# Optimization experiments

Measured on AMD Instinct MI355X. Metric: run time of the kernel, lower is better.

Reference implementation:

```python
import jax, jax.numpy as jnp
import numpy as np

T, N, F, E, P, G, H, B = 8, 40000, 256, 640000, 128, 128, 128, 1024

def setup_inputs() -> dict:
    key = jax.random.key(0)
    ks = jax.random.split(key, 20)
    s = 0.05
    inp = {
        "x": jax.random.normal(ks[0], (T, N, F), jnp.float32),
        "edge_index": jax.random.randint(ks[1], (2, E), 0, N, dtype=jnp.int64),
        "target_indices": jax.random.randint(ks[2], (B,), 0, N, dtype=jnp.int64),
        # projection layer
        "proj_w": jax.random.normal(ks[3], (F, P), jnp.float32) * s,
        "proj_b": jnp.zeros((P,), jnp.float32),
        # GCN layers (weight + bias, symmetric-norm GCNConv with self-loops)
        "gcn_w1": jax.random.normal(ks[4], (P, G), jnp.float32) * s,
        "gcn_b1": jnp.zeros((G,), jnp.float32),
        "gcn_w2": jax.random.normal(ks[5], (G, G), jnp.float32) * s,
        "gcn_b2": jnp.zeros((G,), jnp.float32),
        # GRU (PyTorch layout: [3H, in], gates order r,z,n)
        "gru_w_ih": jax.random.normal(ks[6], (3 * H, 2 * G), jnp.float32) * s,
        "gru_w_hh": jax.random.normal(ks[7], (3 * H, H), jnp.float32) * s,
        "gru_b_ih": jnp.zeros((3 * H,), jnp.float32),
        "gru_b_hh": jnp.zeros((3 * H,), jnp.float32),
        # attention pooling
        "attn_w": jax.random.normal(ks[8], (H, 1), jnp.float32) * s,
        "attn_b": jnp.zeros((1,), jnp.float32),
        # predictor MLP (dropout in eval mode -> identity)
        "pred_w1": jax.random.normal(ks[9], (H, 16), jnp.float32) * s,
        "pred_b1": jnp.zeros((16,), jnp.float32),
        "pred_w2": jax.random.normal(ks[10], (16, 1), jnp.float32) * s,
        "pred_b2": jnp.zeros((1,), jnp.float32),
    }
    return inp


def reference(x, edge_index, target_indices, proj_w, proj_b, gcn_w1, gcn_b1,
              gcn_w2, gcn_b2, gru_w_ih, gru_w_hh, gru_b_ih, gru_b_hh,
              attn_w, attn_b, pred_w1, pred_b1, pred_w2, pred_b2):
    n = x.shape[1]
    # GCNConv normalization: add self-loops, deg^-1/2 A_hat deg^-1/2
    loops = jnp.arange(n, dtype=edge_index.dtype)
    src = jnp.concatenate([edge_index[0], loops])
    dst = jnp.concatenate([edge_index[1], loops])
    deg = jax.ops.segment_sum(jnp.ones_like(src, x.dtype), dst, num_segments=n)
    dinv = jnp.where(deg > 0, jax.lax.rsqrt(deg), 0.0)
    norm = (dinv[src] * dinv[dst])[:, None]  # [E+N, 1]

    def gcn_layer(h, w, b):
        m = h @ w                               # [N, G]
        agg = jax.ops.segment_sum(m[src] * norm, dst, num_segments=n)
        return jax.nn.relu(agg + b)

    def per_step(xt):
        h = jax.nn.relu(xt @ proj_w + proj_b)    # projection
        h1 = gcn_layer(h, gcn_w1, gcn_b1)
        h2 = gcn_layer(h1, gcn_w2, gcn_b2)
        return jnp.concatenate([h1, h2], axis=-1)  # jumping-knowledge concat

    emb = jax.vmap(per_step)(x)                  # [T, N, 2G]
    tgt = emb[:, target_indices]                 # [T, B, 2G]

    hdim = gru_w_hh.shape[1]
    def gru_cell(h, xt):
        gi = xt @ gru_w_ih.T + gru_b_ih
        gh = h @ gru_w_hh.T + gru_b_hh
        ir, iz, ig = jnp.split(gi, 3, axis=-1)
        hr, hz, hg = jnp.split(gh, 3, axis=-1)
        r = jax.nn.sigmoid(ir + hr)
        z = jax.nn.sigmoid(iz + hz)
        g = jnp.tanh(ig + r * hg)
        h_new = (1.0 - z) * g + z * h
        return h_new, h_new

    h0 = jnp.zeros((tgt.shape[1], hdim), x.dtype)
    _, outs = jax.lax.scan(gru_cell, h0, tgt)    # [T, B, H]
    rnn_out = outs.transpose(1, 0, 2)            # [B, T, H]

    scores = jnp.tanh(rnn_out @ attn_w + attn_b)       # [B, T, 1]
    attn_weights = jax.nn.softmax(scores, axis=1)
    rep = jnp.sum(rnn_out * attn_weights, axis=1)      # [B, H]

    hmid = jax.nn.relu(rep @ pred_w1 + pred_b1)        # dropout: eval mode
    pred = hmid @ pred_w2 + pred_b2                    # [B, 1]
    return pred, attn_weights.squeeze(-1)
```

## Files before the change

kernel.cpp:

```cpp
#include <hip/hip_runtime.h>
#include <stdint.h>

#define TT 8
#define NN 40000
#define FF 256
#define EE 640000
#define BB 1024
#define ROWS 320000

typedef __attribute__((ext_vector_type(8))) short s16x8;
typedef __attribute__((ext_vector_type(4))) float f32x4;

__device__ __forceinline__ unsigned short f2bf(float f){
  unsigned int u = __float_as_uint(f);
  u += 0x7fffu + ((u >> 16) & 1u);
  return (unsigned short)(u >> 16);
}
__device__ __forceinline__ float bflo(unsigned int u){ return __uint_as_float(u << 16); }
__device__ __forceinline__ float bfhi(unsigned int u){ return __uint_as_float(u & 0xffff0000u); }

__device__ __forceinline__ void gl2lds16(const void* g, void* l){
  auto gp = reinterpret_cast<const unsigned int __attribute__((address_space(1)))*>(
      reinterpret_cast<uintptr_t>(g));
  auto lp = reinterpret_cast<unsigned int __attribute__((address_space(3)))*>(
      static_cast<unsigned int>(reinterpret_cast<uintptr_t>(l)));
  __builtin_amdgcn_global_load_lds(gp, lp, 16, 0, 0);
}

__global__ void prep_k(const float* __restrict__ proj_w, const float* __restrict__ w1,
                       const float* __restrict__ w2, const float* __restrict__ wih,
                       const float* __restrict__ whh,
                       unsigned short* __restrict__ projwt, unsigned short* __restrict__ w1t,
                       unsigned short* __restrict__ w2t, unsigned short* __restrict__ wihb,
                       uint2* __restrict__ whhp)
{
  int i = blockIdx.x * 256 + threadIdx.x;
  if (i < 32768) {
    int p = i >> 8, f = i & 255;
    projwt[i] = f2bf(proj_w[f * 128 + p]);
  } else if (i < 49152) {
    int k = i - 32768; int o = k >> 7, c = k & 127;
    w1t[k] = f2bf(w1[c * 128 + o]);
  } else if (i < 65536) {
    int k = i - 49152; int o = k >> 7, c = k & 127;
    w2t[k] = f2bf(w2[c * 128 + o]);
  } else if (i < 163840) {
    int k = i - 65536;
    wihb[k] = f2bf(wih[k]);
  } else if (i < 180224) {
    int k = i - 163840; int kk = k >> 7, j = k & 127;
    unsigned int lo = (unsigned int)f2bf(whh[j * 128 + kk]) |
                      ((unsigned int)f2bf(whh[(128 + j) * 128 + kk]) << 16);
    unsigned int hi = (unsigned int)f2bf(whh[(256 + j) * 128 + kk]);
    whhp[k] = make_uint2(lo, hi);
  }
}

__global__ void init_k(int* __restrict__ counts, int* __restrict__ fill){
  int i = blockIdx.x * 256 + threadIdx.x;
  if (i < NN) { counts[i] = 0; fill[i] = 0; }
}
__global__ void count_k(const int* __restrict__ dst, int* __restrict__ counts){
  int i = blockIdx.x * 256 + threadIdx.x;
  if (i < EE) atomicAdd(&counts[dst[i]], 1);
}
__global__ void scan_k(const int* __restrict__ counts, int* __restrict__ rp,
                       float* __restrict__ dinv)
{
  __shared__ int sums[1024];
  const int CH = 40;
  int t = threadIdx.x;
  int beg = t * CH, end = beg + CH; if (end > NN) end = NN; if (beg > NN) beg = NN;
  int s = 0;
  for (int i = beg; i < end; i++) s += counts[i];
  sums[t] = s;
  __syncthreads();
  for (int off = 1; off < 1024; off <<= 1) {
    int add = (t >= off) ? sums[t - off] : 0;
    __syncthreads();
    sums[t] += add;
    __syncthreads();
  }
  int run = sums[t] - s;
  for (int i = beg; i < end; i++) { rp[i] = run; run += counts[i]; }
  if (t == 1023) rp[NN] = sums[1023];
  for (int i = beg; i < end; i++) dinv[i] = rsqrtf((float)(counts[i] + 1));
}
__global__ void fill_k(const int* __restrict__ src, const int* __restrict__ dst,
                       const int* __restrict__ rp, int* __restrict__ fill,
                       int* __restrict__ ci)
{
  int i = blockIdx.x * 256 + threadIdx.x;
  if (i < EE) {
    int d = dst[i];
    int pos = rp[d] + atomicAdd(&fill[d], 1);
    ci[pos] = src[i];
  }
}

template<int MODE>
__global__ __launch_bounds__(256)
void gemm_k(const void* __restrict__ Ap, const short* __restrict__ Bt,
            void* __restrict__ Cp, int K, int ldc,
            const float* __restrict__ dinv)
{
  __shared__ short lA[128 * 64];
  __shared__ short lB[128 * 64];
  const int tid = threadIdx.x;
  const int lane = tid & 63, wave = tid >> 6;
  const int row0 = blockIdx.x * 128;
  const int col0 = blockIdx.y * 128;
  const int qr = (wave & 1) * 64, qc = (wave >> 1) * 64;
  const int m = lane & 15, q = lane >> 4;

  f32x4 acc[4][4];
#pragma unroll
  for (int i = 0; i < 4; i++)
#pragma unroll
    for (int j = 0; j < 4; j++) acc[i][j] = (f32x4){0.f, 0.f, 0.f, 0.f};

  for (int k0 = 0; k0 < K; k0 += 64) {
    __syncthreads();
    {
      const short* A = (const short*)Ap;
#pragma unroll
      for (int i = 0; i < 4; i++) {
        int c = wave * 4 + i;
        int row = c * 8 + (lane >> 3);
        int kg = (lane & 7) ^ (row & 7);
        gl2lds16(A + (size_t)(row0 + row) * K + k0 + kg * 8, lA + c * 512);
      }
    }
#pragma unroll
    for (int i = 0; i < 4; i++) {
      int c = wave * 4 + i;
      int row = c * 8 + (lane >> 3);
      int kg = (lane & 7) ^ (row & 7);
      gl2lds16(Bt + (size_t)(col0 + row) * K + k0 + kg * 8, lB + c * 512);
    }
    __syncthreads();
#pragma unroll
    for (int ks = 0; ks < 2; ks++) {
      s16x8 af[4], bf[4];
#pragma unroll
      for (int i = 0; i < 4; i++) {
        int R = qr + 16 * i + m;
        af[i] = *(const s16x8*)&lA[R * 64 + (((ks * 4 + q) ^ (R & 7)) * 8)];
        int RB = qc + 16 * i + m;
        bf[i] = *(const s16x8*)&lB[RB * 64 + (((ks * 4 + q) ^ (RB & 7)) * 8)];
      }
#pragma unroll
      for (int i = 0; i < 4; i++)
#pragma unroll
        for (int j = 0; j < 4; j++)
          acc[i][j] = __builtin_amdgcn_mfma_f32_16x16x32_bf16(af[i], bf[j], acc[i][j], 0, 0, 0);
    }
  }
#pragma unroll
  for (int i = 0; i < 4; i++) {
    int rbase = row0 + qr + 16 * i + q * 4;
#pragma unroll
    for (int j = 0; j < 4; j++) {
      int col = col0 + qc + 16 * j + m;
#pragma unroll
      for (int rr = 0; rr < 4; rr++) {
        int rg = rbase + rr;
        float v = acc[i][j][rr];
        if (MODE == 1) {
          v *= dinv[rg % NN];
          ((unsigned short*)Cp)[(size_t)rg * ldc + col] = f2bf(v);
        } else {
          ((float*)Cp)[(size_t)rg * ldc + col] = v;
        }
      }
    }
  }
}

__global__ __launch_bounds__(256)
void projgcn_k(const float* __restrict__ x, const short* __restrict__ projwt,
               const short* __restrict__ w1t, const float* __restrict__ proj_b,
               const float* __restrict__ dinv, unsigned short* __restrict__ Ms1)
{
  __shared__ short lds[128 * 64 * 3];
  short* lA = lds;
  short* lB = lds + 8192;
  short* lH = lds + 8192;
  const int tid = threadIdx.x;
  const int lane = tid & 63, wave = tid >> 6;
  const int row0 = blockIdx.x * 128;
  const int qr = (wave & 1) * 64, qc = (wave >> 1) * 64;
  const int m = lane & 15, q = lane >> 4;

  f32x4 acc[4][4];
#pragma unroll
  for (int i = 0; i < 4; i++)
#pragma unroll
    for (int j = 0; j < 4; j++) acc[i][j] = (f32x4){0.f, 0.f, 0.f, 0.f};

  for (int k0 = 0; k0 < 256; k0 += 64) {
    __syncthreads();
    {
      int row = tid >> 1, half = tid & 1;
      const float* gp = x + (size_t)(row0 + row) * 256 + k0 + half * 32;
#pragma unroll
      for (int gi = 0; gi < 4; gi++) {
        float4 v0 = *(const float4*)(gp + gi * 8);
        float4 v1 = *(const float4*)(gp + gi * 8 + 4);
        uint4 w;
        w.x = (unsigned)f2bf(v0.x) | ((unsigned)f2bf(v0.y) << 16);
        w.y = (unsigned)f2bf(v0.z) | ((unsigned)f2bf(v0.w) << 16);
        w.z = (unsigned)f2bf(v1.x) | ((unsigned)f2bf(v1.y) << 16);
        w.w = (unsigned)f2bf(v1.z) | ((unsigned)f2bf(v1.w) << 16);
        int g = half * 4 + gi;
        *(uint4*)&lA[row * 64 + ((g ^ (row & 7)) * 8)] = w;
      }
    }
#pragma unroll
    for (int i = 0; i < 4; i++) {
      int c = wave * 4 + i;
      int row = c * 8 + (lane >> 3);
      int kg = (lane & 7) ^ (row & 7);
      gl2lds16(projwt + (size_t)row * 256 + k0 + kg * 8, lB + c * 512);
    }
    __syncthreads();
#pragma unroll
    for (int ks = 0; ks < 2; ks++) {
      s16x8 af[4], bf[4];
#pragma unroll
      for (int i = 0; i < 4; i++) {
        int R = qr + 16 * i + m;
        af[i] = *(const s16x8*)&lA[R * 64 + (((ks * 4 + q) ^ (R & 7)) * 8)];
        int RB = qc + 16 * i + m;
        bf[i] = *(const s16x8*)&lB[RB * 64 + (((ks * 4 + q) ^ (RB & 7)) * 8)];
      }
#pragma unroll
      for (int i = 0; i < 4; i++)
#pragma unroll
        for (int j = 0; j < 4; j++)
          acc[i][j] = __builtin_amdgcn_mfma_f32_16x16x32_bf16(af[i], bf[j], acc[i][j], 0, 0, 0);
    }
  }
  __syncthreads();

#pragma unroll
  for (int i = 0; i < 4; i++) {
    int rb = qr + 16 * i + q * 4;
#pragma unroll
    for (int j = 0; j < 4; j++) {
      int c = qc + 16 * j + m;
      int chalf = c & 64;
      int gsw = (c >> 3) & 7;
      float bv = proj_b[c];
#pragma unroll
      for (int rr = 0; rr < 4; rr++) {
        int r_loc = rb + rr;
        float v = fmaxf(acc[i][j][rr] + bv, 0.f);
        lH[r_loc * 128 + chalf + ((gsw ^ (r_loc & 7)) << 3) + (c & 7)] = (short)f2bf(v);
      }
      acc[i][j] = (f32x4){0.f, 0.f, 0.f, 0.f};
    }
  }

  for (int k0 = 0; k0 < 128; k0 += 64) {
    __syncthreads();
#pragma unroll
    for (int i = 0; i < 4; i++) {
      int c = wave * 4 + i;
      int row = c * 8 + (lane >> 3);
      int kg = (lane & 7) ^ (row & 7);
      gl2lds16(w1t + (size_t)row * 128 + k0 + kg * 8, lA + c * 512);
    }
    __syncthreads();
#pragma unroll
    for (int ks = 0; ks < 2; ks++) {
      s16x8 af[4], bf[4];
#pragma unroll
      for (int i = 0; i < 4; i++) {
        int R = qr + 16 * i + m;
        af[i] = *(const s16x8*)&lH[R * 128 + k0 + (((ks * 4 + q) ^ (R & 7)) << 3)];
        int RB = qc + 16 * i + m;
        bf[i] = *(const s16x8*)&lA[RB * 64 + (((ks * 4 + q) ^ (RB & 7)) << 3)];
      }
#pragma unroll
      for (int i = 0; i < 4; i++)
#pragma unroll
        for (int j = 0; j < 4; j++)
          acc[i][j] = __builtin_amdgcn_mfma_f32_16x16x32_bf16(af[i], bf[j], acc[i][j], 0, 0, 0);
    }
  }

#pragma unroll
  for (int i = 0; i < 4; i++) {
    int rbase = row0 + qr + 16 * i + q * 4;
#pragma unroll
    for (int j = 0; j < 4; j++) {
      int col = qc + 16 * j + m;
#pragma unroll
      for (int rr = 0; rr < 4; rr++) {
        int rg = rbase + rr;
        float v = acc[i][j][rr] * dinv[rg % NN];
        Ms1[(size_t)rg * 128 + col] = f2bf(v);
      }
    }
  }
}

__global__ __launch_bounds__(256)
void agg_k(const uint2* __restrict__ Ms, uint2* __restrict__ Hout,
           const int* __restrict__ rp, const int* __restrict__ ci,
           const float* __restrict__ dinv, const float* __restrict__ bias)
{
  int widx = blockIdx.x * 4 + (threadIdx.x >> 6);
  int lane = threadIdx.x & 63;
  int li = lane & 31, h = lane >> 5;
  int t = widx / NN;
  int v = widx - t * NN;
  const uint2* base = Ms + (size_t)t * NN * 32 + li;

  uint2 su = base[(size_t)v * 32];
  float a0, a1, a2, a3;
  if (h == 0) { a0 = bflo(su.x); a1 = bfhi(su.x); a2 = bflo(su.y); a3 = bfhi(su.y); }
  else        { a0 = 0.f; a1 = 0.f; a2 = 0.f; a3 = 0.f; }

  int e0 = rp[v], e1 = rp[v + 1];
  for (int chunk = e0; chunk < e1; chunk += 64) {
    int cnt = min(64, e1 - chunk);
    int myIdx = (lane < cnt) ? ci[chunk + lane] : 0;
    int j = 0;
    for (; j + 8 <= cnt; j += 8) {
      int s0 = __shfl(myIdx, j + h, 64);
      int s1 = __shfl(myIdx, j + 2 + h, 64);
      int s2 = __shfl(myIdx, j + 4 + h, 64);
      int s3 = __shfl(myIdx, j + 6 + h, 64);
      uint2 w0 = base[(size_t)s0 * 32];
      uint2 w1 = base[(size_t)s1 * 32];
      uint2 w2 = base[(size_t)s2 * 32];
      uint2 w3 = base[(size_t)s3 * 32];
      a0 += bflo(w0.x) + bflo(w1.x) + bflo(w2.x) + bflo(w3.x);
      a1 += bfhi(w0.x) + bfhi(w1.x) + bfhi(w2.x) + bfhi(w3.x);
      a2 += bflo(w0.y) + bflo(w1.y) + bflo(w2.y) + bflo(w3.y);
      a3 += bfhi(w0.y) + bfhi(w1.y) + bfhi(w2.y) + bfhi(w3.y);
    }
    for (; j + 2 <= cnt; j += 2) {
      int s = __shfl(myIdx, j + h, 64);
      uint2 w = base[(size_t)s * 32];
      a0 += bflo(w.x); a1 += bfhi(w.x); a2 += bflo(w.y); a3 += bfhi(w.y);
    }
    if (j < cnt) {
      int s = __shfl(myIdx, j, 64);
      if (h == 0) {
        uint2 w = base[(size_t)s * 32];
        a0 += bflo(w.x); a1 += bfhi(w.x); a2 += bflo(w.y); a3 += bfhi(w.y);
      }
    }
  }
  a0 += __shfl_xor(a0, 32, 64);
  a1 += __shfl_xor(a1, 32, 64);
  a2 += __shfl_xor(a2, 32, 64);
  a3 += __shfl_xor(a3, 32, 64);
  if (h == 0) {
    float dv = dinv[v];
    float r0 = fmaxf(fmaf(dv, a0, bias[li * 4 + 0]), 0.f);
    float r1 = fmaxf(fmaf(dv, a1, bias[li * 4 + 1]), 0.f);
    float r2 = fmaxf(fmaf(dv, a2, bias[li * 4 + 2]), 0.f);
    float r3 = fmaxf(fmaf(dv, a3, bias[li * 4 + 3]), 0.f);
    uint2 o;
    o.x = (unsigned)f2bf(r0) | ((unsigned)f2bf(r1) << 16);
    o.y = (unsigned)f2bf(r2) | ((unsigned)f2bf(r3) << 16);
    Hout[(size_t)widx * 32 + li] = o;
  }
}

__global__ void gather_k(const unsigned int* __restrict__ h1, const unsigned int* __restrict__ h2,
                         const int* __restrict__ tix, unsigned int* __restrict__ TGT)
{
  int i = blockIdx.x * 256 + threadIdx.x;
  int dw = i & 127; int r = i >> 7; int b = r & 1023; int t = r >> 10;
  int node = tix[b];
  size_t src = ((size_t)t * NN + node) * 64 + (dw & 63);
  unsigned int val = (dw < 64) ? h1[src] : h2[src];
  TGT[(size_t)r * 128 + dw] = val;
}

__global__ __launch_bounds__(256)
void gru_attn_k(const float* __restrict__ GI, const uint2* __restrict__ Whp,
                const float* __restrict__ b_ih, const float* __restrict__ b_hh,
                const float* __restrict__ attw, const float* __restrict__ attb,
                float* __restrict__ rep, float* __restrict__ out_attn)
{
  __shared__ float hbuf[2][128];
  __shared__ float red[2][2];
  __shared__ float sc[2][8];
  int tid = threadIdx.x;
  int r = tid >> 7, j = tid & 127;
  int lane = tid & 63, wv = tid >> 6;
  int b = blockIdx.x * 2 + r;
  hbuf[r][j] = 0.f;
  float bi0 = b_ih[j], bi1 = b_ih[128 + j], bi2 = b_ih[256 + j];
  float bh0 = b_hh[j], bh1 = b_hh[128 + j], bh2 = b_hh[256 + j];
  float aw = attw[j], ab = attb[0];
  float ht[8];
  __syncthreads();
  for (int t = 0; t < 8; t++) {
    const float* gi = GI + ((size_t)(t * 1024 + b)) * 384;
    float accr = bh0, accz = bh1, accg = bh2;
#pragma unroll 4
    for (int k = 0; k < 128; k++) {
      float hk = hbuf[r][k];
      uint2 wp = Whp[k * 128 + j];
      accr += hk * bflo(wp.x);
      accz += hk * bfhi(wp.x);
      accg += hk * bflo(wp.y);
    }
    float x0 = gi[j] + bi0, x1 = gi[128 + j] + bi1, x2 = gi[256 + j] + bi2;
    float rg = 1.f / (1.f + __expf(-(x0 + accr)));
    float z  = 1.f / (1.f + __expf(-(x1 + accz)));
    float g  = tanhf(x2 + rg * accg);
    float hp = hbuf[r][j];
    float hn = (1.f - z) * g + z * hp;
    __syncthreads();
    hbuf[r][j] = hn;
    float p = hn * aw;
    for (int off = 32; off; off >>= 1) p += __shfl_down(p, off, 64);
    if (lane == 0) red[wv >> 1][wv & 1] = p;
    __syncthreads();
    if (j == 0) sc[r][t] = tanhf(red[r][0] + red[r][1] + ab);
    ht[t] = hn;
  }
  __syncthreads();
  float s[8], mx = -1e30f;
#pragma unroll
  for (int t = 0; t < 8; t++) { s[t] = sc[r][t]; mx = fmaxf(mx, s[t]); }
  float sum = 0.f;
#pragma unroll
  for (int t = 0; t < 8; t++) { s[t] = __expf(s[t] - mx); sum += s[t]; }
  float inv = 1.f / sum;
  float rv = 0.f;
#pragma unroll
  for (int t = 0; t < 8; t++) rv += s[t] * inv * ht[t];
  rep[(size_t)b * 128 + j] = rv;
  if (j < 8) out_attn[b * 8 + j] = s[j] * inv;
}

__global__ void pred_k(const float* __restrict__ rep, const float* __restrict__ w1,
                       const float* __restrict__ b1, const float* __restrict__ w2,
                       const float* __restrict__ b2, float* __restrict__ out)
{
  int bidx = blockIdx.x * 256 + threadIdx.x;
  if (bidx >= 1024) return;
  const float* rp = rep + (size_t)bidx * 128;
  float acc[16];
#pragma unroll
  for (int i = 0; i < 16; i++) acc[i] = b1[i];
  for (int k = 0; k < 128; k++) {
    float rv = rp[k];
#pragma unroll
    for (int i = 0; i < 16; i++) acc[i] += rv * w1[k * 16 + i];
  }
  float pv = b2[0];
#pragma unroll
  for (int i = 0; i < 16; i++) pv += fmaxf(acc[i], 0.f) * w2[i];
  out[bidx] = pv;
}

extern "C" void kernel_launch(void* const* d_in, const int* in_sizes, int n_in,
                              void* d_out, int out_size, void* d_ws, size_t ws_size,
                              hipStream_t stream)
{
  (void)in_sizes; (void)n_in; (void)out_size; (void)ws_size;
  const float* x      = (const float*)d_in[0];
  const int*   ei     = (const int*)d_in[1];
  const int*   tix    = (const int*)d_in[2];
  const float* proj_w = (const float*)d_in[3];
  const float* proj_b = (const float*)d_in[4];
  const float* gcn_w1 = (const float*)d_in[5];
  const float* gcn_b1 = (const float*)d_in[6];
  const float* gcn_w2 = (const float*)d_in[7];
  const float* gcn_b2 = (const float*)d_in[8];
  const float* w_ih   = (const float*)d_in[9];
  const float* w_hh   = (const float*)d_in[10];
  const float* b_ih   = (const float*)d_in[11];
  const float* b_hh   = (const float*)d_in[12];
  const float* attw   = (const float*)d_in[13];
  const float* attb   = (const float*)d_in[14];
  const float* pw1    = (const float*)d_in[15];
  const float* pb1    = (const float*)d_in[16];
  const float* pw2    = (const float*)d_in[17];
  const float* pb2    = (const float*)d_in[18];
  float* out = (float*)d_out;

  char* ws = (char*)d_ws;
  size_t off = 0;
  auto alloc = [&](size_t bytes) -> char* {
    char* p = ws + off; off += (bytes + 255) & ~(size_t)255; return p;
  };
  int*   counts = (int*)alloc((size_t)NN * 4);
  int*   fill   = (int*)alloc((size_t)NN * 4);
  int*   rp     = (int*)alloc((size_t)(NN + 1) * 4);
  float* dinv   = (float*)alloc((size_t)NN * 4);
  int*   ci     = (int*)alloc((size_t)EE * 4);
  unsigned short* projwt = (unsigned short*)alloc(128 * 256 * 2);
  unsigned short* w1t    = (unsigned short*)alloc(128 * 128 * 2);
  unsigned short* w2t    = (unsigned short*)alloc(128 * 128 * 2);
  unsigned short* wihb   = (unsigned short*)alloc(384 * 256 * 2);
  uint2* whhp            = (uint2*)alloc(128 * 128 * 8);
  unsigned int* TGT = (unsigned int*)alloc((size_t)8192 * 256 * 2);
  float* GI  = (float*)alloc((size_t)8192 * 384 * 4);
  float* rep = (float*)alloc((size_t)1024 * 128 * 4);
  unsigned short* bufA = (unsigned short*)alloc((size_t)ROWS * 128 * 2);
  unsigned short* bufB = (unsigned short*)alloc((size_t)ROWS * 128 * 2);
  unsigned short* bufC = (unsigned short*)alloc((size_t)ROWS * 128 * 2);

  const int* e_src = ei;
  const int* e_dst = ei + EE;

  prep_k<<<704, 256, 0, stream>>>(proj_w, gcn_w1, gcn_w2, w_ih, w_hh,
                                  projwt, w1t, w2t, wihb, whhp);
  init_k<<<157, 256, 0, stream>>>(counts, fill);
  count_k<<<2500, 256, 0, stream>>>(e_dst, counts);
  scan_k<<<1, 1024, 0, stream>>>(counts, rp, dinv);
  fill_k<<<2500, 256, 0, stream>>>(e_src, e_dst, rp, fill, ci);

  projgcn_k<<<2500, 256, 0, stream>>>(x, (const short*)projwt, (const short*)w1t,
                                      proj_b, dinv, bufB);
  agg_k<<<80000, 256, 0, stream>>>((const uint2*)bufB, (uint2*)bufC,
                                   rp, ci, dinv, gcn_b1);
  gemm_k<1><<<dim3(2500, 1), 256, 0, stream>>>(bufC, (const short*)w2t, bufB,
                                               128, 128, dinv);
  agg_k<<<80000, 256, 0, stream>>>((const uint2*)bufB, (uint2*)bufA,
                                   rp, ci, dinv, gcn_b2);
  gather_k<<<4096, 256, 0, stream>>>((const unsigned int*)bufC, (const unsigned int*)bufA,
                                     tix, TGT);
  gemm_k<2><<<dim3(64, 3), 256, 0, stream>>>(TGT, (const short*)wihb, GI,
                                             256, 384, nullptr);
  gru_attn_k<<<512, 256, 0, stream>>>(GI, whhp, b_ih, b_hh, attw, attb, rep, out + 1024);
  pred_k<<<4, 256, 0, stream>>>(rep, pw1, pb1, pw2, pb2, out);
}
```

Measured before the change: 1.172 ms.

## Widen aggregation loads to 16 bytes and fuse gather, init, and predictor kernels

The sparse aggregation kernel now has 16 lanes each load a 16-byte (8 bf16) slice of a row, so a wave processes four neighbours per step instead of two. The target-row gather is folded into the GRU input GEMM through indexed global-to-LDS loads, which removes the TGT buffer and one launch. The counter init is merged into the prep kernel, and the prediction MLP is merged into the GRU/attention kernel. The wider loads cut the number of memory instructions in the dominant aggregation pass, but the extra shuffle reduction stages and the remainder handling add some overhead.

```diff
diff --git a/kernel.cpp b/kernel.cpp
--- a/kernel.cpp
+++ b/kernel.cpp
@@ -32,9 +32,10 @@
                        const float* __restrict__ whh,
                        unsigned short* __restrict__ projwt, unsigned short* __restrict__ w1t,
                        unsigned short* __restrict__ w2t, unsigned short* __restrict__ wihb,
-                       uint2* __restrict__ whhp)
+                       uint2* __restrict__ whhp, int* __restrict__ counts, int* __restrict__ fill)
 {
   int i = blockIdx.x * 256 + threadIdx.x;
+  if (i < NN) { counts[i] = 0; fill[i] = 0; }
   if (i < 32768) {
     int p = i >> 8, f = i & 255;
     projwt[i] = f2bf(proj_w[f * 128 + p]);
@@ -56,10 +57,6 @@
   }
 }
 
-__global__ void init_k(int* __restrict__ counts, int* __restrict__ fill){
-  int i = blockIdx.x * 256 + threadIdx.x;
-  if (i < NN) { counts[i] = 0; fill[i] = 0; }
-}
 __global__ void count_k(const int* __restrict__ dst, int* __restrict__ counts){
   int i = blockIdx.x * 256 + threadIdx.x;
   if (i < EE) atomicAdd(&counts[dst[i]], 1);
@@ -98,11 +95,12 @@
   }
 }
 
-template<int MODE>
+template<int MODE, int GIA>
 __global__ __launch_bounds__(256)
 void gemm_k(const void* __restrict__ Ap, const short* __restrict__ Bt,
             void* __restrict__ Cp, int K, int ldc,
-            const float* __restrict__ dinv)
+            const float* __restrict__ dinv,
+            const short* __restrict__ A2, const int* __restrict__ tix)
 {
   __shared__ short lA[128 * 64];
   __shared__ short lB[128 * 64];
@@ -121,7 +119,20 @@
 
   for (int k0 = 0; k0 < K; k0 += 64) {
     __syncthreads();
-    {
+    if (GIA) {
+      const short* h1p = (const short*)Ap;
+#pragma unroll
+      for (int i = 0; i < 4; i++) {
+        int c = wave * 4 + i;
+        int row = c * 8 + (lane >> 3);
+        int kg = (lane & 7) ^ (row & 7);
+        int r = row0 + row;
+        int tt = r >> 10, bb = r & 1023;
+        int node = tix[bb];
+        const short* srcp = (k0 < 128) ? h1p : A2;
+        gl2lds16(srcp + ((size_t)tt * NN + node) * 128 + (k0 & 127) + kg * 8, lA + c * 512);
+      }
+    } else {
       const short* A = (const short*)Ap;
 #pragma unroll
       for (int i = 0; i < 4; i++) {
@@ -307,87 +318,98 @@
 }
 
 __global__ __launch_bounds__(256)
-void agg_k(const uint2* __restrict__ Ms, uint2* __restrict__ Hout,
+void agg_k(const uint4* __restrict__ Ms, uint4* __restrict__ Hout,
            const int* __restrict__ rp, const int* __restrict__ ci,
            const float* __restrict__ dinv, const float* __restrict__ bias)
 {
   int widx = blockIdx.x * 4 + (threadIdx.x >> 6);
   int lane = threadIdx.x & 63;
-  int li = lane & 31, h = lane >> 5;
+  int li = lane & 15, g = lane >> 4;
   int t = widx / NN;
   int v = widx - t * NN;
-  const uint2* base = Ms + (size_t)t * NN * 32 + li;
-
-  uint2 su = base[(size_t)v * 32];
-  float a0, a1, a2, a3;
-  if (h == 0) { a0 = bflo(su.x); a1 = bfhi(su.x); a2 = bflo(su.y); a3 = bfhi(su.y); }
-  else        { a0 = 0.f; a1 = 0.f; a2 = 0.f; a3 = 0.f; }
+  const uint4* base = Ms + (size_t)t * NN * 16 + li;
+
+  float a0 = 0.f, a1 = 0.f, a2 = 0.f, a3 = 0.f, a4 = 0.f, a5 = 0.f, a6 = 0.f, a7 = 0.f;
+  if (g == 0) {
+    uint4 su = base[(size_t)v * 16];
+    a0 = bflo(su.x); a1 = bfhi(su.x); a2 = bflo(su.y); a3 = bfhi(su.y);
+    a4 = bflo(su.z); a5 = bfhi(su.z); a6 = bflo(su.w); a7 = bfhi(su.w);
+  }
 
   int e0 = rp[v], e1 = rp[v + 1];
   for (int chunk = e0; chunk < e1; chunk += 64) {
     int cnt = min(64, e1 - chunk);
     int myIdx = (lane < cnt) ? ci[chunk + lane] : 0;
     int j = 0;
-    for (; j + 8 <= cnt; j += 8) {
-      int s0 = __shfl(myIdx, j + h, 64);
-      int s1 = __shfl(myIdx, j + 2 + h, 64);
-      int s2 = __shfl(myIdx, j + 4 + h, 64);
-      int s3 = __shfl(myIdx, j + 6 + h, 64);
-      uint2 w0 = base[(size_t)s0 * 32];
-      uint2 w1 = base[(size_t)s1 * 32];
-      uint2 w2 = base[(size_t)s2 * 32];
-      uint2 w3 = base[(size_t)s3 * 32];
+    for (; j + 16 <= cnt; j += 16) {
+      int s0 = __shfl(myIdx, j + g, 64);
+      int s1 = __shfl(myIdx, j + 4 + g, 64);
+      int s2 = __shfl(myIdx, j + 8 + g, 64);
+      int s3 = __shfl(myIdx, j + 12 + g, 64);
+      uint4 w0 = base[(size_t)s0 * 16];
+      uint4 w1 = base[(size_t)s1 * 16];
+      uint4 w2 = base[(size_t)s2 * 16];
+      uint4 w3 = base[(size_t)s3 * 16];
       a0 += bflo(w0.x) + bflo(w1.x) + bflo(w2.x) + bflo(w3.x);
       a1 += bfhi(w0.x) + bfhi(w1.x) + bfhi(w2.x) + bfhi(w3.x);
       a2 += bflo(w0.y) + bflo(w1.y) + bflo(w2.y) + bflo(w3.y);
       a3 += bfhi(w0.y) + bfhi(w1.y) + bfhi(w2.y) + bfhi(w3.y);
-    }
-    for (; j + 2 <= cnt; j += 2) {
-      int s = __shfl(myIdx, j + h, 64);
-      uint2 w = base[(size_t)s * 32];
+      a4 += bflo(w0.z) + bflo(w1.z) + bflo(w2.z) + bflo(w3.z);
+      a5 += bfhi(w0.z) + bfhi(w1.z) + bfhi(w2.z) + bfhi(w3.z);
+      a6 += bflo(w0.w) + bflo(w1.w) + bflo(w2.w) + bflo(w3.w);
+      a7 += bfhi(w0.w) + bfhi(w1.w) + bfhi(w2.w) + bfhi(w3.w);
+    }
+    for (; j + 4 <= cnt; j += 4) {
+      int s = __shfl(myIdx, j + g, 64);
+      uint4 w = base[(size_t)s * 16];
       a0 += bflo(w.x); a1 += bfhi(w.x); a2 += bflo(w.y); a3 += bfhi(w.y);
-    }
-    if (j < cnt) {
-      int s = __shfl(myIdx, j, 64);
-      if (h == 0) {
-        uint2 w = base[(size_t)s * 32];
+      a4 += bflo(w.z); a5 += bfhi(w.z); a6 += bflo(w.w); a7 += bfhi(w.w);
+    }
+    int rem = cnt - j;
+    if (rem > 0) {
+      int sidx = j + g; if (sidx >= cnt) sidx = j;
+      int s = __shfl(myIdx, sidx, 64);
+      if (g < rem) {
+        uint4 w = base[(size_t)s * 16];
         a0 += bflo(w.x); a1 += bfhi(w.x); a2 += bflo(w.y); a3 += bfhi(w.y);
-      }
-    }
-  }
-  a0 += __shfl_xor(a0, 32, 64);
-  a1 += __shfl_xor(a1, 32, 64);
-  a2 += __shfl_xor(a2, 32, 64);
-  a3 += __shfl_xor(a3, 32, 64);
-  if (h == 0) {
+        a4 += bflo(w.z); a5 += bfhi(w.z); a6 += bflo(w.w); a7 += bfhi(w.w);
+      }
+    }
+  }
+  a0 += __shfl_xor(a0, 16, 64); a0 += __shfl_xor(a0, 32, 64);
+  a1 += __shfl_xor(a1, 16, 64); a1 += __shfl_xor(a1, 32, 64);
+  a2 += __shfl_xor(a2, 16, 64); a2 += __shfl_xor(a2, 32, 64);
+  a3 += __shfl_xor(a3, 16, 64); a3 += __shfl_xor(a3, 32, 64);
+  a4 += __shfl_xor(a4, 16, 64); a4 += __shfl_xor(a4, 32, 64);
+  a5 += __shfl_xor(a5, 16, 64); a5 += __shfl_xor(a5, 32, 64);
+  a6 += __shfl_xor(a6, 16, 64); a6 += __shfl_xor(a6, 32, 64);
+  a7 += __shfl_xor(a7, 16, 64); a7 += __shfl_xor(a7, 32, 64);
+  if (g == 0) {
     float dv = dinv[v];
-    float r0 = fmaxf(fmaf(dv, a0, bias[li * 4 + 0]), 0.f);
-    float r1 = fmaxf(fmaf(dv, a1, bias[li * 4 + 1]), 0.f);
-    float r2 = fmaxf(fmaf(dv, a2, bias[li * 4 + 2]), 0.f);
-    float r3 = fmaxf(fmaf(dv, a3, bias[li * 4 + 3]), 0.f);
-    uint2 o;
+    float r0 = fmaxf(fmaf(dv, a0, bias[li * 8 + 0]), 0.f);
+    float r1 = fmaxf(fmaf(dv, a1, bias[li * 8 + 1]), 0.f);
+    float r2 = fmaxf(fmaf(dv, a2, bias[li * 8 + 2]), 0.f);
+    float r3 = fmaxf(fmaf(dv, a3, bias[li * 8 + 3]), 0.f);
+    float r4 = fmaxf(fmaf(dv, a4, bias[li * 8 + 4]), 0.f);
+    float r5 = fmaxf(fmaf(dv, a5, bias[li * 8 + 5]), 0.f);
+    float r6 = fmaxf(fmaf(dv, a6, bias[li * 8 + 6]), 0.f);
+    float r7 = fmaxf(fmaf(dv, a7, bias[li * 8 + 7]), 0.f);
+    uint4 o;
     o.x = (unsigned)f2bf(r0) | ((unsigned)f2bf(r1) << 16);
     o.y = (unsigned)f2bf(r2) | ((unsigned)f2bf(r3) << 16);
-    Hout[(size_t)widx * 32 + li] = o;
-  }
-}
-
-__global__ void gather_k(const unsigned int* __restrict__ h1, const unsigned int* __restrict__ h2,
-                         const int* __restrict__ tix, unsigned int* __restrict__ TGT)
-{
-  int i = blockIdx.x * 256 + threadIdx.x;
-  int dw = i & 127; int r = i >> 7; int b = r & 1023; int t = r >> 10;
-  int node = tix[b];
-  size_t src = ((size_t)t * NN + node) * 64 + (dw & 63);
-  unsigned int val = (dw < 64) ? h1[src] : h2[src];
-  TGT[(size_t)r * 128 + dw] = val;
+    o.z = (unsigned)f2bf(r4) | ((unsigned)f2bf(r5) << 16);
+    o.w = (unsigned)f2bf(r6) | ((unsigned)f2bf(r7) << 16);
+    Hout[(size_t)widx * 16 + li] = o;
+  }
 }
 
 __global__ __launch_bounds__(256)
 void gru_attn_k(const float* __restrict__ GI, const uint2* __restrict__ Whp,
                 const float* __restrict__ b_ih, const float* __restrict__ b_hh,
                 const float* __restrict__ attw, const float* __restrict__ attb,
-                float* __restrict__ rep, float* __restrict__ out_attn)
+                const float* __restrict__ pw1, const float* __restrict__ pb1,
+                const float* __restrict__ pw2, const float* __restrict__ pb2,
+                float* __restrict__ out)
 {
   __shared__ float hbuf[2][128];
   __shared__ float red[2][2];
@@ -439,29 +461,20 @@
   float rv = 0.f;
 #pragma unroll
   for (int t = 0; t < 8; t++) rv += s[t] * inv * ht[t];
-  rep[(size_t)b * 128 + j] = rv;
-  if (j < 8) out_attn[b * 8 + j] = s[j] * inv;
-}
-
-__global__ void pred_k(const float* __restrict__ rep, const float* __restrict__ w1,
-                       const float* __restrict__ b1, const float* __restrict__ w2,
-                       const float* __restrict__ b2, float* __restrict__ out)
-{
-  int bidx = blockIdx.x * 256 + threadIdx.x;
-  if (bidx >= 1024) return;
-  const float* rp = rep + (size_t)bidx * 128;
-  float acc[16];
-#pragma unroll
-  for (int i = 0; i < 16; i++) acc[i] = b1[i];
-  for (int k = 0; k < 128; k++) {
-    float rv = rp[k];
-#pragma unroll
-    for (int i = 0; i < 16; i++) acc[i] += rv * w1[k * 16 + i];
-  }
-  float pv = b2[0];
-#pragma unroll
-  for (int i = 0; i < 16; i++) pv += fmaxf(acc[i], 0.f) * w2[i];
-  out[bidx] = pv;
+  if (j < 8) out[1024 + b * 8 + j] = s[j] * inv;
+  hbuf[r][j] = rv;
+  __syncthreads();
+  if (j < 16) {
+    float acc = pb1[j];
+#pragma unroll 4
+    for (int k = 0; k < 128; k++) acc += hbuf[r][k] * pw1[k * 16 + j];
+    float p = fmaxf(acc, 0.f) * pw2[j];
+    p += __shfl_down(p, 8, 64);
+    p += __shfl_down(p, 4, 64);
+    p += __shfl_down(p, 2, 64);
+    p += __shfl_down(p, 1, 64);
+    if (j == 0) out[b] = p + pb2[0];
+  }
 }
 
 extern "C" void kernel_launch(void* const* d_in, const int* in_sizes, int n_in,
@@ -505,9 +518,7 @@
   unsigned short* w2t    = (unsigned short*)alloc(128 * 128 * 2);
   unsigned short* wihb   = (unsigned short*)alloc(384 * 256 * 2);
   uint2* whhp            = (uint2*)alloc(128 * 128 * 8);
-  unsigned int* TGT = (unsigned int*)alloc((size_t)8192 * 256 * 2);
   float* GI  = (float*)alloc((size_t)8192 * 384 * 4);
-  float* rep = (float*)alloc((size_t)1024 * 128 * 4);
   unsigned short* bufA = (unsigned short*)alloc((size_t)ROWS * 128 * 2);
   unsigned short* bufB = (unsigned short*)alloc((size_t)ROWS * 128 * 2);
   unsigned short* bufC = (unsigned short*)alloc((size_t)ROWS * 128 * 2);
@@ -516,24 +527,22 @@
   const int* e_dst = ei + EE;
 
   prep_k<<<704, 256, 0, stream>>>(proj_w, gcn_w1, gcn_w2, w_ih, w_hh,
-                                  projwt, w1t, w2t, wihb, whhp);
-  init_k<<<157, 256, 0, stream>>>(counts, fill);
+                                  projwt, w1t, w2t, wihb, whhp, counts, fill);
   count_k<<<2500, 256, 0, stream>>>(e_dst, counts);
   scan_k<<<1, 1024, 0, stream>>>(counts, rp, dinv);
   fill_k<<<2500, 256, 0, stream>>>(e_src, e_dst, rp, fill, ci);
 
   projgcn_k<<<2500, 256, 0, stream>>>(x, (const short*)projwt, (const short*)w1t,
                                       proj_b, dinv, bufB);
-  agg_k<<<80000, 256, 0, stream>>>((const uint2*)bufB, (uint2*)bufC,
+  agg_k<<<80000, 256, 0, stream>>>((const uint4*)bufB, (uint4*)bufC,
                                    rp, ci, dinv, gcn_b1);
-  gemm_k<1><<<dim3(2500, 1), 256, 0, stream>>>(bufC, (const short*)w2t, bufB,
-                                               128, 128, dinv);
-  agg_k<<<80000, 256, 0, stream>>>((const uint2*)bufB, (uint2*)bufA,
+  gemm_k<1, 0><<<dim3(2500, 1), 256, 0, stream>>>(bufC, (const short*)w2t, bufB,
+                                                  128, 128, dinv, nullptr, nullptr);
+  agg_k<<<80000, 256, 0, stream>>>((const uint4*)bufB, (uint4*)bufA,
                                    rp, ci, dinv, gcn_b2);
-  gather_k<<<4096, 256, 0, stream>>>((const unsigned int*)bufC, (const unsigned int*)bufA,
-                                     tix, TGT);
-  gemm_k<2><<<dim3(64, 3), 256, 0, stream>>>(TGT, (const short*)wihb, GI,
-                                             256, 384, nullptr);
-  gru_attn_k<<<512, 256, 0, stream>>>(GI, whhp, b_ih, b_hh, attw, attb, rep, out + 1024);
-  pred_k<<<4, 256, 0, stream>>>(rep, pw1, pb1, pw2, pb2, out);
-}
+  gemm_k<2, 1><<<dim3(64, 3), 256, 0, stream>>>(bufC, (const short*)wihb, GI,
+                                                256, 384, nullptr,
+                                                (const short*)bufA, (const int*)tix);
+  gru_attn_k<<<512, 256, 0, stream>>>(GI, whhp, b_ih, b_hh, attw, attb,
+                                      pw1, pb1, pw2, pb2, out);
+}
```

Result: faster. 1.142 ms (-2.6%).
